# Kernel optimization log

Hardware: AMD Instinct MI355X
Metric: run time of the kernel (lower is better)

The kernel has to match this reference:

```python
import jax, jax.numpy as jnp
from jax import lax
import numpy as np

B, T = 2, 4096
NQ, NAUX, NR, NS, K = 256, 28, 512, 256, 2
DIL = [2 ** i for i in range(10)] * 3  # 30 residual blocks
L = len(DIL)


def _causal_conv(x, w, b, d):
    # x: (B, Cin, T), w: (Cout, Cin, K) -- left-pad (K-1)*d for causality
    pad = (w.shape[-1] - 1) * d
    y = lax.conv_general_dilated(x, w, window_strides=(1,), padding=[(pad, 0)],
                                 rhs_dilation=(d,),
                                 dimension_numbers=('NCH', 'OIH', 'NCH'))
    return y + b[None, :, None]


def _conv1x1(x, w, b):
    # x: (B, Cin, T), w: (Cout, Cin)
    return jnp.einsum('oc,bct->bot', w, x) + b[None, :, None]


def setup_inputs() -> dict:
    key = jax.random.key(0)
    ks = jax.random.split(key, 32)
    s = 0.05
    n = lambda k, shp: (jax.random.normal(k, shp, dtype=jnp.float32) * s)
    return {
        'x': jax.random.randint(ks[0], (B, T), 0, NQ, dtype=jnp.int32),
        'h': jax.random.normal(ks[1], (B, NAUX, T), dtype=jnp.float32),
        'causal_w': n(ks[2], (NR, NQ, K)), 'causal_b': n(ks[3], (NR,)),
        'dil_sig_w': n(ks[4], (L, NR, NR, K)), 'dil_sig_b': n(ks[5], (L, NR)),
        'dil_tanh_w': n(ks[6], (L, NR, NR, K)), 'dil_tanh_b': n(ks[7], (L, NR)),
        'aux_sig_w': n(ks[8], (L, NR, NAUX)), 'aux_sig_b': n(ks[9], (L, NR)),
        'aux_tanh_w': n(ks[10], (L, NR, NAUX)), 'aux_tanh_b': n(ks[11], (L, NR)),
        'skip_w': n(ks[12], (L, NS, NR)), 'skip_b': n(ks[13], (L, NS)),
        'res_w': n(ks[14], (L, NR, NR)), 'res_b': n(ks[15], (L, NR)),
        'post1_w': n(ks[16], (NS, NS)), 'post1_b': n(ks[17], (NS,)),
        'post2_w': n(ks[18], (NQ, NS)), 'post2_b': n(ks[19], (NQ,)),
        'lin_w': n(ks[20], (NQ, NQ)), 'lin_b': n(ks[21], (NQ,)),
    }


def reference(x, h, causal_w, causal_b, dil_sig_w, dil_sig_b, dil_tanh_w,
              dil_tanh_b, aux_sig_w, aux_sig_b, aux_tanh_w, aux_tanh_b,
              skip_w, skip_b, res_w, res_b, post1_w, post1_b, post2_w,
              post2_b, lin_w, lin_b):
    # preprocess: one-hot -> (B, NQ, T) -> causal conv
    oh = jax.nn.one_hot(x % NQ, NQ, dtype=jnp.float32).transpose(0, 2, 1)
    out = _causal_conv(oh, causal_w, causal_b, 1)  # (B, NR, T)
    skip_sum = jnp.zeros((B, NS, T), dtype=jnp.float32)
    for l, d in enumerate(DIL):
        s = _causal_conv(out, dil_sig_w[l], dil_sig_b[l], d) \
            + _conv1x1(h, aux_sig_w[l], aux_sig_b[l])
        t = _causal_conv(out, dil_tanh_w[l], dil_tanh_b[l], d) \
            + _conv1x1(h, aux_tanh_w[l], aux_tanh_b[l])
        g = jax.nn.sigmoid(s) * jnp.tanh(t)  # gated activation (B, NR, T)
        skip_sum = skip_sum + _conv1x1(g, skip_w[l], skip_b[l])
        out = _conv1x1(g, res_w[l], res_b[l]) + out  # residual
    o = jax.nn.relu(skip_sum)
    o = jax.nn.relu(_conv1x1(o, post1_w, post1_b))
    o = _conv1x1(o, post2_w, post2_b).transpose(0, 2, 1)  # (B, T, NQ)
    return o @ lin_w.T + lin_b
```

## Files before the change

kernel.cpp:

```cpp
#include <hip/hip_runtime.h>
#include <cstddef>

#define B_ 2
#define T_ 4096
#define NQ_ 256
#define NAUX_ 28
#define NR_ 512
#define NS_ 256
#define L_ 30

typedef _Float16 half_t;
typedef __attribute__((ext_vector_type(8))) _Float16 f16x8;
typedef __attribute__((ext_vector_type(4))) _Float16 f16x4;
typedef __attribute__((ext_vector_type(4))) float f32x4;

__device__ inline half_t f2h(float f) { return (half_t)f; }
__device__ inline float h2f(half_t h) { return (float)h; }

__device__ __forceinline__ void gload16(const void* g, void* l) {
    __builtin_amdgcn_global_load_lds(
        (const __attribute__((address_space(1))) unsigned int*)g,
        (__attribute__((address_space(3))) unsigned int*)l, 16, 0, 0);
}

__global__ __launch_bounds__(256) void gates_gemm(
    const half_t* __restrict__ actB, const half_t* __restrict__ Wg,
    const float* __restrict__ biasG, half_t* __restrict__ g,
    const half_t* __restrict__ zbuf, int dil)
{
    __shared__ __align__(16) half_t sA[128 * 64];
    __shared__ __align__(16) half_t sB[128 * 64];

    const int tid = threadIdx.x;
    const int b = blockIdx.z;
    const int tB = blockIdx.x * 128;
    const int mB = blockIdx.y * 128;
    const int w = tid >> 6, lane = tid & 63;
    const int wm = w >> 1, wn = w & 1;
    const int l15 = lane & 15, lg = lane >> 4;
    const int rr = lane >> 3, cc = lane & 7;
    const int sc8 = cc ^ rr;

    f32x4 acc[4][4] = {};

    const half_t* Wb = Wg + (size_t)mB * 1088;

    for (int kc = 0; kc < 17; kc++) {
#pragma unroll
        for (int it = 0; it < 4; it++) {
            const int row = w * 32 + it * 8 + rr;
            gload16(Wb + (size_t)row * 1088 + kc * 64 + sc8 * 8,
                    &sA[(w * 32 + it * 8) * 64]);
        }
#pragma unroll
        for (int it = 0; it < 4; it++) {
            const int t = tB + w * 32 + it * 8 + rr;
            const half_t* p;
            if (kc < 8) {
                p = actB + ((size_t)b * T_ + t) * 576 + kc * 64;
            } else if (kc < 16) {
                const int tp = t - dil;
                p = (tp >= 0) ? actB + ((size_t)b * T_ + tp) * 576 + (kc - 8) * 64
                              : zbuf;
            } else {
                p = actB + ((size_t)b * T_ + t) * 576 + 512;
            }
            gload16(p + sc8 * 8, &sB[(w * 32 + it * 8) * 64]);
        }
        __syncthreads();
#pragma unroll
        for (int s = 0; s < 2; s++) {
            f16x8 av[4], bv[4];
#pragma unroll
            for (int i = 0; i < 4; i++) {
                const int r = wm * 64 + i * 16 + l15;
                av[i] = *(const f16x8*)&sA[r * 64 + (((s * 4 + lg) ^ (l15 & 7)) * 8)];
            }
#pragma unroll
            for (int j = 0; j < 4; j++) {
                const int r = wn * 64 + j * 16 + l15;
                bv[j] = *(const f16x8*)&sB[r * 64 + (((s * 4 + lg) ^ (l15 & 7)) * 8)];
            }
#pragma unroll
            for (int i = 0; i < 4; i++)
#pragma unroll
                for (int j = 0; j < 4; j++)
                    acc[i][j] = __builtin_amdgcn_mfma_f32_16x16x32_f16(av[i], bv[j], acc[i][j], 0, 0, 0);
        }
        __syncthreads();
    }

    const int gidx = blockIdx.y * 2 + wm;
    const int t0 = tB + wn * 64 + l15;
#pragma unroll
    for (int i = 0; i < 2; i++) {
        const int c = gidx * 32 + i * 16 + lg * 4;
        const float4 bs = *(const float4*)&biasG[gidx * 64 + i * 16 + lg * 4];
        const float4 bt4 = *(const float4*)&biasG[gidx * 64 + 32 + i * 16 + lg * 4];
        const float bsa[4] = {bs.x, bs.y, bs.z, bs.w};
        const float bta[4] = {bt4.x, bt4.y, bt4.z, bt4.w};
#pragma unroll
        for (int j = 0; j < 4; j++) {
            const int t = t0 + j * 16;
            f16x4 o;
#pragma unroll
            for (int e = 0; e < 4; e++) {
                const float sv = acc[i][j][e] + bsa[e];
                const float tv = acc[i + 2][j][e] + bta[e];
                const float sg = 1.f / (1.f + __expf(-sv));
                const float ex = __expf(-2.f * tv);
                const float th = (1.f - ex) / (1.f + ex);
                o[e] = f2h(sg * th);
            }
            *(f16x4*)(g + ((size_t)b * T_ + t) * 512 + c) = o;
        }
    }
}

template<int EPI>
__global__ __launch_bounds__(256) void gemm_mfma(
    const half_t* __restrict__ X, const half_t* __restrict__ W,
    const float* __restrict__ bias, void* __restrict__ out, int M, int K,
    half_t* __restrict__ actB, half_t* __restrict__ skipH)
{
    __shared__ __align__(16) half_t sA[128 * 64];
    __shared__ __align__(16) half_t sB[128 * 64];

    const int tid = threadIdx.x;
    const int b = blockIdx.z;
    const int tB = blockIdx.x * 128;
    const int mB = blockIdx.y * 128;
    const int w = tid >> 6, lane = tid & 63;
    const int wm = w >> 1, wn = w & 1;
    const int l15 = lane & 15, lg = lane >> 4;
    const int rr = lane >> 3, cc = lane & 7;
    const int sc8 = cc ^ rr;

    f32x4 acc[4][4] = {};

    const half_t* Xb = X + ((size_t)b * T_ + tB) * K;
    const half_t* Wb = W + (size_t)mB * K;

    const int nk = K >> 6;
    for (int kc = 0; kc < nk; kc++) {
        const int k0 = kc << 6;
#pragma unroll
        for (int it = 0; it < 4; it++) {
            const int row = w * 32 + it * 8 + rr;
            gload16(Wb + (size_t)row * K + k0 + sc8 * 8, &sA[(w * 32 + it * 8) * 64]);
            gload16(Xb + (size_t)row * K + k0 + sc8 * 8, &sB[(w * 32 + it * 8) * 64]);
        }
        __syncthreads();
#pragma unroll
        for (int s = 0; s < 2; s++) {
            f16x8 av[4], bv[4];
#pragma unroll
            for (int i = 0; i < 4; i++) {
                const int r = wm * 64 + i * 16 + l15;
                av[i] = *(const f16x8*)&sA[r * 64 + (((s * 4 + lg) ^ (l15 & 7)) * 8)];
            }
#pragma unroll
            for (int j = 0; j < 4; j++) {
                const int r = wn * 64 + j * 16 + l15;
                bv[j] = *(const f16x8*)&sB[r * 64 + (((s * 4 + lg) ^ (l15 & 7)) * 8)];
            }
#pragma unroll
            for (int i = 0; i < 4; i++)
#pragma unroll
                for (int j = 0; j < 4; j++)
                    acc[i][j] = __builtin_amdgcn_mfma_f32_16x16x32_f16(av[i], bv[j], acc[i][j], 0, 0, 0);
        }
        __syncthreads();
    }

    const int n0 = tB + wn * 64 + l15;
#pragma unroll
    for (int i = 0; i < 4; i++) {
        const int m = mB + wm * 64 + i * 16 + lg * 4;
        float4 bv = make_float4(0.f, 0.f, 0.f, 0.f);
        if (bias) bv = *(const float4*)&bias[m];
#pragma unroll
        for (int j = 0; j < 4; j++) {
            const int t = n0 + j * 16;
            float o0 = acc[i][j][0] + bv.x, o1 = acc[i][j][1] + bv.y;
            float o2 = acc[i][j][2] + bv.z, o3 = acc[i][j][3] + bv.w;
            if (EPI == 1) {
                o0 = fmaxf(o0, 0.f); o1 = fmaxf(o1, 0.f);
                o2 = fmaxf(o2, 0.f); o3 = fmaxf(o3, 0.f);
            }
            if (EPI == 3) {
                const size_t bt = (size_t)b * T_ + t;
                half_t* p = (mB < 512) ? (actB + bt * 576 + m)
                                       : (skipH + bt * 256 + (m - 512));
                f16x4 old = *(const f16x4*)p;
                f16x4 nv = {f2h(h2f(old.x) + o0), f2h(h2f(old.y) + o1),
                            f2h(h2f(old.z) + o2), f2h(h2f(old.w) + o3)};
                *(f16x4*)p = nv;
            } else {
                const size_t off = ((size_t)b * T_ + t) * M + m;
                if (EPI == 2) {
                    *(float4*)((float*)out + off) = make_float4(o0, o1, o2, o3);
                } else {
                    f16x4 ov = {f2h(o0), f2h(o1), f2h(o2), f2h(o3)};
                    *(f16x4*)((half_t*)out + off) = ov;
                }
            }
        }
    }
}

__global__ __launch_bounds__(256) void relupack_kernel(
    const half_t* __restrict__ skipH, half_t* __restrict__ outp)
{
    const int idx = blockIdx.x * 256 + threadIdx.x;
    const int c = (idx & 63) * 4;
    const int bt = idx >> 6;
    const f16x4 v = *(const f16x4*)(skipH + (size_t)bt * 256 + c);
    f16x4 o = {f2h(fmaxf(h2f(v.x), 0.f)), f2h(fmaxf(h2f(v.y), 0.f)),
               f2h(fmaxf(h2f(v.z), 0.f)), f2h(fmaxf(h2f(v.w), 0.f))};
    *(f16x4*)(outp + (size_t)bt * 256 + c) = o;
}

__global__ __launch_bounds__(256) void embed_kernel(
    const int* __restrict__ x, const float* __restrict__ cw,
    const float* __restrict__ cb, half_t* __restrict__ actB)
{
    const int t = blockIdx.x, b = blockIdx.y;
    const int idc = x[b * T_ + t];
    const int idp = (t > 0) ? x[b * T_ + t - 1] : -1;
    const size_t bt = (size_t)b * T_ + t;
    for (int c = threadIdx.x; c < 512; c += 256) {
        float v = cw[(c * 256 + idc) * 2 + 1] + cb[c];
        if (idp >= 0) v += cw[(c * 256 + idp) * 2 + 0];
        actB[bt * 576 + c] = f2h(v);
    }
}

__global__ __launch_bounds__(256) void packh_kernel(
    const float* __restrict__ h, half_t* __restrict__ actB)
{
    const int idx = blockIdx.x * 256 + threadIdx.x;
    const int j = idx & 63;
    const int bt = idx >> 6;
    const int b = bt >> 12, t = bt & 4095;
    const float v = (j < 28) ? h[((size_t)b * NAUX_ + j) * T_ + t] : 0.f;
    actB[(size_t)bt * 576 + 512 + j] = f2h(v);
}

__global__ __launch_bounds__(256) void packgate_kernel(
    const float* __restrict__ dsw, const float* __restrict__ dtw,
    half_t* __restrict__ Wg)
{
    const int idx = blockIdx.x * 256 + threadIdx.x;
    const int kg = idx & 63;
    const int r = (idx >> 6) & 1023;
    const int l = idx >> 16;
    const int rsub = r & 63;
    const int c = (r >> 6) * 32 + (rsub & 31);
    const float* src = (rsub < 32) ? dsw : dtw;
    const int k0 = kg * 8;
    const float4* p = (const float4*)(src + (((size_t)l * 512 + c) * 512 + k0) * 2);
    const float4 q0 = p[0], q1 = p[1], q2 = p[2], q3 = p[3];
    f16x8 cur = {f2h(q0.y), f2h(q0.w), f2h(q1.y), f2h(q1.w),
                 f2h(q2.y), f2h(q2.w), f2h(q3.y), f2h(q3.w)};
    f16x8 pst = {f2h(q0.x), f2h(q0.z), f2h(q1.x), f2h(q1.z),
                 f2h(q2.x), f2h(q2.z), f2h(q3.x), f2h(q3.z)};
    half_t* row = Wg + ((size_t)l * 1024 + r) * 1088;
    *(f16x8*)&row[k0] = cur;
    *(f16x8*)&row[512 + k0] = pst;
}

__global__ __launch_bounds__(256) void packgaux_kernel(
    const float* __restrict__ asw, const float* __restrict__ atw,
    half_t* __restrict__ Wg)
{
    const int idx = blockIdx.x * 256 + threadIdx.x;
    const int j8 = idx & 7;
    const int r = (idx >> 3) & 1023;
    const int l = idx >> 13;
    const int rsub = r & 63;
    const int c = (r >> 6) * 32 + (rsub & 31);
    const float* src = (rsub < 32) ? asw : atw;
    f16x8 v = {};
#pragma unroll
    for (int e = 0; e < 8; e++) {
        const int j = j8 * 8 + e;
        if (j < NAUX_) v[e] = f2h(src[((size_t)l * 512 + c) * NAUX_ + j]);
    }
    *(f16x8*)&Wg[((size_t)l * 1024 + r) * 1088 + 1024 + j8 * 8] = v;
}

__global__ __launch_bounds__(256) void packsr_kernel(
    const float* __restrict__ rsw, const float* __restrict__ skw,
    half_t* __restrict__ Wsr)
{
    const int idx = blockIdx.x * 256 + threadIdx.x;
    const int c = (idx & 127) * 4;
    const int r = (idx >> 7) % 768;
    const int l = idx / (128 * 768);
    const float4 v = (r < 512)
        ? *(const float4*)&rsw[((size_t)l * 512 + r) * 512 + c]
        : *(const float4*)&skw[((size_t)l * 256 + (r - 512)) * 512 + c];
    f16x4 o = {f2h(v.x), f2h(v.y), f2h(v.z), f2h(v.w)};
    *(f16x4*)(Wsr + ((size_t)l * 768 + r) * 512 + c) = o;
}

__global__ __launch_bounds__(256) void packpost_kernel(
    const float* __restrict__ p1w, const float* __restrict__ p2w,
    const float* __restrict__ lw, half_t* __restrict__ Wpost)
{
    const int idx = blockIdx.x * 256 + threadIdx.x;
    const int c = (idx & 63) * 4;
    const int r = (idx >> 6) & 255;
    const int mi = idx >> 14;
    const float* src = (mi == 0) ? p1w : (mi == 1) ? p2w : lw;
    const float4 v = *(const float4*)&src[(size_t)r * 256 + c];
    f16x4 o = {f2h(v.x), f2h(v.y), f2h(v.z), f2h(v.w)};
    *(f16x4*)(Wpost + (size_t)mi * 65536 + (size_t)r * 256 + c) = o;
}

__global__ __launch_bounds__(256) void packbias_kernel(
    const float* __restrict__ dsb, const float* __restrict__ asb,
    const float* __restrict__ dtb, const float* __restrict__ atb,
    const float* __restrict__ rsb, const float* __restrict__ skb,
    float* __restrict__ biasG, float* __restrict__ biasSr)
{
    const int idx = blockIdx.x * 256 + threadIdx.x;
    if (idx < 30 * 1024) {
        const int l = idx >> 10, r = idx & 1023;
        const int rsub = r & 63;
        const int c = (r >> 6) * 32 + (rsub & 31);
        const float v = (rsub < 32) ? (dsb[l * 512 + c] + asb[l * 512 + c])
                                    : (dtb[l * 512 + c] + atb[l * 512 + c]);
        biasG[idx] = v;
    } else if (idx < 30 * 1024 + 30 * 768) {
        const int j = idx - 30 * 1024;
        const int l = j / 768, r = j % 768;
        biasSr[j] = (r < 512) ? rsb[l * 512 + r] : skb[l * 256 + (r - 512)];
    }
}

extern "C" void kernel_launch(void* const* d_in, const int* in_sizes, int n_in,
                              void* d_out, int out_size, void* d_ws, size_t ws_size,
                              hipStream_t stream)
{
    (void)in_sizes; (void)n_in; (void)out_size; (void)ws_size;

    const int* x = (const int*)d_in[0];
    const float* h = (const float*)d_in[1];
    const float* causal_w = (const float*)d_in[2];
    const float* causal_b = (const float*)d_in[3];
    const float* dsw = (const float*)d_in[4];
    const float* dsb = (const float*)d_in[5];
    const float* dtw = (const float*)d_in[6];
    const float* dtb = (const float*)d_in[7];
    const float* asw = (const float*)d_in[8];
    const float* asb = (const float*)d_in[9];
    const float* atw = (const float*)d_in[10];
    const float* atb = (const float*)d_in[11];
    const float* skw = (const float*)d_in[12];
    const float* skb = (const float*)d_in[13];
    const float* rsw = (const float*)d_in[14];
    const float* rsb = (const float*)d_in[15];
    const float* p1w = (const float*)d_in[16];
    const float* p1b = (const float*)d_in[17];
    const float* p2w = (const float*)d_in[18];
    const float* p2b = (const float*)d_in[19];
    const float* lw  = (const float*)d_in[20];
    const float* lb  = (const float*)d_in[21];

    char* ws = (char*)d_ws;
    size_t off = 0;
    auto alloc = [&](size_t bytes) { char* p = ws + off; off += (bytes + 255) & ~(size_t)255; return p; };

    half_t* Wg     = (half_t*)alloc((size_t)L_ * 1024 * 1088 * 2);
    half_t* Wsr    = (half_t*)alloc((size_t)L_ * 768 * 512 * 2);
    half_t* Wpost  = (half_t*)alloc((size_t)3 * 256 * 256 * 2);
    float*  biasG  = (float*) alloc((size_t)L_ * 1024 * 4);
    float*  biasSr = (float*) alloc((size_t)L_ * 768 * 4);
    half_t* actB   = (half_t*)alloc((size_t)B_ * T_ * 576 * 2);
    half_t* g      = (half_t*)alloc((size_t)B_ * T_ * 512 * 2);
    half_t* skipH  = (half_t*)alloc((size_t)B_ * T_ * 256 * 2);
    half_t* zbuf   = (half_t*)alloc(256);
    half_t* pA     = (half_t*)alloc((size_t)B_ * T_ * 256 * 2);
    half_t* pB     = (half_t*)alloc((size_t)B_ * T_ * 256 * 2);

    hipMemsetAsync(skipH, 0, (size_t)B_ * T_ * 256 * 2 + 256, stream);

    packgate_kernel<<<30 * 1024 * 64 / 256, 256, 0, stream>>>(dsw, dtw, Wg);
    packgaux_kernel<<<30 * 1024 * 8 / 256, 256, 0, stream>>>(asw, atw, Wg);
    packsr_kernel<<<30 * 768 * 128 / 256, 256, 0, stream>>>(rsw, skw, Wsr);
    packpost_kernel<<<3 * 256 * 64 / 256, 256, 0, stream>>>(p1w, p2w, lw, Wpost);
    packbias_kernel<<<(30 * 1024 + 30 * 768 + 255) / 256, 256, 0, stream>>>(
        dsb, asb, dtb, atb, rsb, skb, biasG, biasSr);
    packh_kernel<<<B_ * T_ * 64 / 256, 256, 0, stream>>>(h, actB);
    embed_kernel<<<dim3(T_, B_), 256, 0, stream>>>(x, causal_w, causal_b, actB);

    for (int l = 0; l < L_; l++) {
        const int dil = 1 << (l % 10);
        gates_gemm<<<dim3(32, 8, B_), 256, 0, stream>>>(
            actB, Wg + (size_t)l * 1024 * 1088, biasG + (size_t)l * 1024, g, zbuf, dil);
        gemm_mfma<3><<<dim3(32, 6, B_), 256, 0, stream>>>(
            g, Wsr + (size_t)l * 768 * 512, biasSr + (size_t)l * 768, nullptr, 768, 512,
            actB, skipH);
    }

    relupack_kernel<<<B_ * T_ * 64 / 256, 256, 0, stream>>>(skipH, pA);
    gemm_mfma<1><<<dim3(32, 2, B_), 256, 0, stream>>>(pA, Wpost, p1b, pB, 256, 256,
                                                      nullptr, nullptr);
    gemm_mfma<0><<<dim3(32, 2, B_), 256, 0, stream>>>(pB, Wpost + 65536, p2b, pA, 256, 256,
                                                      nullptr, nullptr);
    gemm_mfma<2><<<dim3(32, 2, B_), 256, 0, stream>>>(pA, Wpost + 131072, lb, d_out, 256, 256,
                                                      nullptr, nullptr);
}
```

Before: 1.550 ms.

## Pre-pack weights in MFMA fragment order, load A to registers, double-buffer B

Weight matrices are repacked at setup into a per-lane MFMA fragment layout, so each wave loads its A operands straight from global memory into registers with coalesced 16-byte loads. This removes the A tile from LDS entirely. The activation tile in LDS is now double-buffered, with the next chunk's A and B loads issued before the current chunk's compute, giving one sync per k-step and overlap of loads with MFMA. Launch bounds request two blocks per CU, and K becomes a template parameter. The cost is higher register pressure from the two A register sets, plus repeated global reads of weights across blocks that now rely on cache instead of LDS sharing.

Result: no change. 1.524 ms (-1.7%).

```diff
diff --git a/kernel.cpp b/kernel.cpp
--- a/kernel.cpp
+++ b/kernel.cpp
@@ -23,18 +23,17 @@
         (__attribute__((address_space(3))) unsigned int*)l, 16, 0, 0);
 }
 
-__global__ __launch_bounds__(256) void gates_gemm(
-    const half_t* __restrict__ actB, const half_t* __restrict__ Wg,
+
+__global__ __launch_bounds__(256, 2) void gates_gemm(
+    const half_t* __restrict__ actB, const half_t* __restrict__ Wf,
     const float* __restrict__ biasG, half_t* __restrict__ g,
     const half_t* __restrict__ zbuf, int dil)
 {
-    __shared__ __align__(16) half_t sA[128 * 64];
-    __shared__ __align__(16) half_t sB[128 * 64];
+    __shared__ __align__(16) half_t sB[2][128 * 64];
 
     const int tid = threadIdx.x;
     const int b = blockIdx.z;
     const int tB = blockIdx.x * 128;
-    const int mB = blockIdx.y * 128;
     const int w = tid >> 6, lane = tid & 63;
     const int wm = w >> 1, wn = w & 1;
     const int l15 = lane & 15, lg = lane >> 4;
@@ -42,16 +41,18 @@
     const int sc8 = cc ^ rr;
 
     f32x4 acc[4][4] = {};
-
-    const half_t* Wb = Wg + (size_t)mB * 1088;
-
-    for (int kc = 0; kc < 17; kc++) {
-#pragma unroll
-        for (int it = 0; it < 4; it++) {
-            const int row = w * 32 + it * 8 + rr;
-            gload16(Wb + (size_t)row * 1088 + kc * 64 + sc8 * 8,
-                    &sA[(w * 32 + it * 8) * 64]);
-        }
+    f16x8 a0[8], a1[8];
+
+    const int mgW = blockIdx.y * 8 + wm * 4;
+
+    auto loadA = [&](f16x8* d, int kc) {
+#pragma unroll
+        for (int i = 0; i < 4; i++)
+#pragma unroll
+            for (int s = 0; s < 2; s++)
+                d[i * 2 + s] = *(const f16x8*)&Wf[((size_t)(mgW + i) * 34 + kc * 2 + s) * 512 + lane * 8];
+    };
+    auto stageB = [&](int kc, int buf) {
 #pragma unroll
         for (int it = 0; it < 4; it++) {
             const int t = tB + w * 32 + it * 8 + rr;
@@ -65,29 +66,36 @@
             } else {
                 p = actB + ((size_t)b * T_ + t) * 576 + 512;
             }
-            gload16(p + sc8 * 8, &sB[(w * 32 + it * 8) * 64]);
-        }
-        __syncthreads();
+            gload16(p + sc8 * 8, &sB[buf][(w * 32 + it * 8) * 64]);
+        }
+    };
+    auto compute = [&](const f16x8* a, int buf) {
 #pragma unroll
         for (int s = 0; s < 2; s++) {
-            f16x8 av[4], bv[4];
-#pragma unroll
-            for (int i = 0; i < 4; i++) {
-                const int r = wm * 64 + i * 16 + l15;
-                av[i] = *(const f16x8*)&sA[r * 64 + (((s * 4 + lg) ^ (l15 & 7)) * 8)];
-            }
+            f16x8 bv[4];
 #pragma unroll
             for (int j = 0; j < 4; j++) {
                 const int r = wn * 64 + j * 16 + l15;
-                bv[j] = *(const f16x8*)&sB[r * 64 + (((s * 4 + lg) ^ (l15 & 7)) * 8)];
+                bv[j] = *(const f16x8*)&sB[buf][r * 64 + (((s * 4 + lg) ^ (l15 & 7)) * 8)];
             }
 #pragma unroll
             for (int i = 0; i < 4; i++)
 #pragma unroll
                 for (int j = 0; j < 4; j++)
-                    acc[i][j] = __builtin_amdgcn_mfma_f32_16x16x32_f16(av[i], bv[j], acc[i][j], 0, 0, 0);
-        }
+                    acc[i][j] = __builtin_amdgcn_mfma_f32_16x16x32_f16(a[i * 2 + s], bv[j], acc[i][j], 0, 0, 0);
+        }
+    };
+
+    stageB(0, 0);
+    loadA(a0, 0);
+#pragma unroll
+    for (int kc = 0; kc < 17; kc++) {
         __syncthreads();
+        if (kc + 1 < 17) {
+            stageB(kc + 1, (kc + 1) & 1);
+            loadA((kc & 1) ? a0 : a1, kc + 1);
+        }
+        compute((kc & 1) ? a1 : a0, kc & 1);
     }
 
     const int gidx = blockIdx.y * 2 + wm;
@@ -117,14 +125,15 @@
     }
 }
 
-template<int EPI>
-__global__ __launch_bounds__(256) void gemm_mfma(
-    const half_t* __restrict__ X, const half_t* __restrict__ W,
-    const float* __restrict__ bias, void* __restrict__ out, int M, int K,
+template<int K, int EPI>
+__global__ __launch_bounds__(256, 2) void gemm_mfma(
+    const half_t* __restrict__ X, const half_t* __restrict__ Wf,
+    const float* __restrict__ bias, void* __restrict__ out, int M,
     half_t* __restrict__ actB, half_t* __restrict__ skipH)
 {
-    __shared__ __align__(16) half_t sA[128 * 64];
-    __shared__ __align__(16) half_t sB[128 * 64];
+    constexpr int NK = K / 64;
+    constexpr int NKS = K / 32;
+    __shared__ __align__(16) half_t sB[2][128 * 64];
 
     const int tid = threadIdx.x;
     const int b = blockIdx.z;
@@ -137,40 +146,53 @@
     const int sc8 = cc ^ rr;
 
     f32x4 acc[4][4] = {};
-
+    f16x8 a0[8], a1[8];
+
+    const int mgW = (mB >> 4) + wm * 4;
     const half_t* Xb = X + ((size_t)b * T_ + tB) * K;
-    const half_t* Wb = W + (size_t)mB * K;
-
-    const int nk = K >> 6;
-    for (int kc = 0; kc < nk; kc++) {
-        const int k0 = kc << 6;
+
+    auto loadA = [&](f16x8* d, int kc) {
+#pragma unroll
+        for (int i = 0; i < 4; i++)
+#pragma unroll
+            for (int s = 0; s < 2; s++)
+                d[i * 2 + s] = *(const f16x8*)&Wf[((size_t)(mgW + i) * NKS + kc * 2 + s) * 512 + lane * 8];
+    };
+    auto stageB = [&](int kc, int buf) {
 #pragma unroll
         for (int it = 0; it < 4; it++) {
-            const int row = w * 32 + it * 8 + rr;
-            gload16(Wb + (size_t)row * K + k0 + sc8 * 8, &sA[(w * 32 + it * 8) * 64]);
-            gload16(Xb + (size_t)row * K + k0 + sc8 * 8, &sB[(w * 32 + it * 8) * 64]);
-        }
-        __syncthreads();
+            const int row = w * 32 + it * 8;
+            gload16(Xb + (size_t)(row + rr) * K + kc * 64 + sc8 * 8,
+                    &sB[buf][row * 64]);
+        }
+    };
+    auto compute = [&](const f16x8* a, int buf) {
 #pragma unroll
         for (int s = 0; s < 2; s++) {
-            f16x8 av[4], bv[4];
-#pragma unroll
-            for (int i = 0; i < 4; i++) {
-                const int r = wm * 64 + i * 16 + l15;
-                av[i] = *(const f16x8*)&sA[r * 64 + (((s * 4 + lg) ^ (l15 & 7)) * 8)];
-            }
+            f16x8 bv[4];
 #pragma unroll
             for (int j = 0; j < 4; j++) {
                 const int r = wn * 64 + j * 16 + l15;
-                bv[j] = *(const f16x8*)&sB[r * 64 + (((s * 4 + lg) ^ (l15 & 7)) * 8)];
+                bv[j] = *(const f16x8*)&sB[buf][r * 64 + (((s * 4 + lg) ^ (l15 & 7)) * 8)];
             }
 #pragma unroll
             for (int i = 0; i < 4; i++)
 #pragma unroll
                 for (int j = 0; j < 4; j++)
-                    acc[i][j] = __builtin_amdgcn_mfma_f32_16x16x32_f16(av[i], bv[j], acc[i][j], 0, 0, 0);
-        }
+                    acc[i][j] = __builtin_amdgcn_mfma_f32_16x16x32_f16(a[i * 2 + s], bv[j], acc[i][j], 0, 0, 0);
+        }
+    };
+
+    stageB(0, 0);
+    loadA(a0, 0);
+#pragma unroll
+    for (int kc = 0; kc < NK; kc++) {
         __syncthreads();
+        if (kc + 1 < NK) {
+            stageB(kc + 1, (kc + 1) & 1);
+            loadA((kc & 1) ? a0 : a1, kc + 1);
+        }
+        compute((kc & 1) ? a1 : a0, kc & 1);
     }
 
     const int n0 = tB + wn * 64 + l15;
@@ -252,22 +274,24 @@
     half_t* __restrict__ Wg)
 {
     const int idx = blockIdx.x * 256 + threadIdx.x;
-    const int kg = idx & 63;
-    const int r = (idx >> 6) & 1023;
+    const int lane = idx & 63;
+    const int ks = (idx >> 6) & 15;
+    const int mg = (idx >> 10) & 63;
     const int l = idx >> 16;
+    const int r = mg * 16 + (lane & 15);
     const int rsub = r & 63;
     const int c = (r >> 6) * 32 + (rsub & 31);
     const float* src = (rsub < 32) ? dsw : dtw;
-    const int k0 = kg * 8;
-    const float4* p = (const float4*)(src + (((size_t)l * 512 + c) * 512 + k0) * 2);
+    const size_t base = ((size_t)(l * 512 + c) * 512 + ks * 32 + (lane >> 4) * 8) * 2;
+    const float4* p = (const float4*)(src + base);
     const float4 q0 = p[0], q1 = p[1], q2 = p[2], q3 = p[3];
     f16x8 cur = {f2h(q0.y), f2h(q0.w), f2h(q1.y), f2h(q1.w),
                  f2h(q2.y), f2h(q2.w), f2h(q3.y), f2h(q3.w)};
     f16x8 pst = {f2h(q0.x), f2h(q0.z), f2h(q1.x), f2h(q1.z),
                  f2h(q2.x), f2h(q2.z), f2h(q3.x), f2h(q3.z)};
-    half_t* row = Wg + ((size_t)l * 1024 + r) * 1088;
-    *(f16x8*)&row[k0] = cur;
-    *(f16x8*)&row[512 + k0] = pst;
+    half_t* dst = Wg + (size_t)l * 1114112;
+    *(f16x8*)&dst[((size_t)(mg * 34 + ks) * 64 + lane) * 8] = cur;
+    *(f16x8*)&dst[((size_t)(mg * 34 + 16 + ks) * 64 + lane) * 8] = pst;
 }
 
 __global__ __launch_bounds__(256) void packgaux_kernel(
@@ -275,19 +299,23 @@
     half_t* __restrict__ Wg)
 {
     const int idx = blockIdx.x * 256 + threadIdx.x;
-    const int j8 = idx & 7;
-    const int r = (idx >> 3) & 1023;
+    const int lane = idx & 63;
+    const int ksd = (idx >> 6) & 1;
+    const int mg = (idx >> 7) & 63;
     const int l = idx >> 13;
+    const int r = mg * 16 + (lane & 15);
     const int rsub = r & 63;
     const int c = (r >> 6) * 32 + (rsub & 31);
     const float* src = (rsub < 32) ? asw : atw;
+    const int j0 = ksd * 32 + (lane >> 4) * 8;
     f16x8 v = {};
 #pragma unroll
     for (int e = 0; e < 8; e++) {
-        const int j = j8 * 8 + e;
-        if (j < NAUX_) v[e] = f2h(src[((size_t)l * 512 + c) * NAUX_ + j]);
-    }
-    *(f16x8*)&Wg[((size_t)l * 1024 + r) * 1088 + 1024 + j8 * 8] = v;
+        const int j = j0 + e;
+        if (j < NAUX_) v[e] = f2h(src[(size_t)(l * 512 + c) * NAUX_ + j]);
+    }
+    Wg += (size_t)l * 1114112;
+    *(f16x8*)&Wg[((size_t)(mg * 34 + 32 + ksd) * 64 + lane) * 8] = v;
 }
 
 __global__ __launch_bounds__(256) void packsr_kernel(
@@ -295,14 +323,18 @@
     half_t* __restrict__ Wsr)
 {
     const int idx = blockIdx.x * 256 + threadIdx.x;
-    const int c = (idx & 127) * 4;
-    const int r = (idx >> 7) % 768;
-    const int l = idx / (128 * 768);
-    const float4 v = (r < 512)
-        ? *(const float4*)&rsw[((size_t)l * 512 + r) * 512 + c]
-        : *(const float4*)&skw[((size_t)l * 256 + (r - 512)) * 512 + c];
-    f16x4 o = {f2h(v.x), f2h(v.y), f2h(v.z), f2h(v.w)};
-    *(f16x4*)(Wsr + ((size_t)l * 768 + r) * 512 + c) = o;
+    const int lane = idx & 63;
+    const int ks = (idx >> 6) & 15;
+    const int mg = (idx >> 10) % 48;
+    const int l = (idx >> 10) / 48;
+    const int r = mg * 16 + (lane & 15);
+    const int kb = ks * 32 + (lane >> 4) * 8;
+    const float* src = (r < 512) ? (rsw + ((size_t)l * 512 + r) * 512 + kb)
+                                 : (skw + ((size_t)l * 256 + (r - 512)) * 512 + kb);
+    const float4 q0 = ((const float4*)src)[0], q1 = ((const float4*)src)[1];
+    f16x8 v = {f2h(q0.x), f2h(q0.y), f2h(q0.z), f2h(q0.w),
+               f2h(q1.x), f2h(q1.y), f2h(q1.z), f2h(q1.w)};
+    *(f16x8*)&Wsr[(size_t)l * 393216 + ((size_t)(mg * 16 + ks) * 64 + lane) * 8] = v;
 }
 
 __global__ __launch_bounds__(256) void packpost_kernel(
@@ -310,13 +342,18 @@
     const float* __restrict__ lw, half_t* __restrict__ Wpost)
 {
     const int idx = blockIdx.x * 256 + threadIdx.x;
-    const int c = (idx & 63) * 4;
-    const int r = (idx >> 6) & 255;
-    const int mi = idx >> 14;
+    const int lane = idx & 63;
+    const int ks = (idx >> 6) & 7;
+    const int mg = (idx >> 9) & 15;
+    const int mi = idx >> 13;
     const float* src = (mi == 0) ? p1w : (mi == 1) ? p2w : lw;
-    const float4 v = *(const float4*)&src[(size_t)r * 256 + c];
-    f16x4 o = {f2h(v.x), f2h(v.y), f2h(v.z), f2h(v.w)};
-    *(f16x4*)(Wpost + (size_t)mi * 65536 + (size_t)r * 256 + c) = o;
+    const int r = mg * 16 + (lane & 15);
+    const int kb = ks * 32 + (lane >> 4) * 8;
+    const float4 q0 = ((const float4*)(src + (size_t)r * 256 + kb))[0];
+    const float4 q1 = ((const float4*)(src + (size_t)r * 256 + kb))[1];
+    f16x8 v = {f2h(q0.x), f2h(q0.y), f2h(q0.z), f2h(q0.w),
+               f2h(q1.x), f2h(q1.y), f2h(q1.z), f2h(q1.w)};
+    *(f16x8*)&Wpost[(size_t)mi * 65536 + ((size_t)(mg * 8 + ks) * 64 + lane) * 8] = v;
 }
 
 __global__ __launch_bounds__(256) void packbias_kernel(
@@ -373,9 +410,9 @@
     size_t off = 0;
     auto alloc = [&](size_t bytes) { char* p = ws + off; off += (bytes + 255) & ~(size_t)255; return p; };
 
-    half_t* Wg     = (half_t*)alloc((size_t)L_ * 1024 * 1088 * 2);
-    half_t* Wsr    = (half_t*)alloc((size_t)L_ * 768 * 512 * 2);
-    half_t* Wpost  = (half_t*)alloc((size_t)3 * 256 * 256 * 2);
+    half_t* Wg     = (half_t*)alloc((size_t)L_ * 1114112 * 2);
+    half_t* Wsr    = (half_t*)alloc((size_t)L_ * 393216 * 2);
+    half_t* Wpost  = (half_t*)alloc((size_t)3 * 65536 * 2);
     float*  biasG  = (float*) alloc((size_t)L_ * 1024 * 4);
     float*  biasSr = (float*) alloc((size_t)L_ * 768 * 4);
     half_t* actB   = (half_t*)alloc((size_t)B_ * T_ * 576 * 2);
@@ -387,10 +424,10 @@
 
     hipMemsetAsync(skipH, 0, (size_t)B_ * T_ * 256 * 2 + 256, stream);
 
-    packgate_kernel<<<30 * 1024 * 64 / 256, 256, 0, stream>>>(dsw, dtw, Wg);
-    packgaux_kernel<<<30 * 1024 * 8 / 256, 256, 0, stream>>>(asw, atw, Wg);
-    packsr_kernel<<<30 * 768 * 128 / 256, 256, 0, stream>>>(rsw, skw, Wsr);
-    packpost_kernel<<<3 * 256 * 64 / 256, 256, 0, stream>>>(p1w, p2w, lw, Wpost);
+    packgate_kernel<<<30 * 64 * 16 * 64 / 256, 256, 0, stream>>>(dsw, dtw, Wg);
+    packgaux_kernel<<<30 * 64 * 2 * 64 / 256, 256, 0, stream>>>(asw, atw, Wg);
+    packsr_kernel<<<30 * 48 * 16 * 64 / 256, 256, 0, stream>>>(rsw, skw, Wsr);
+    packpost_kernel<<<3 * 16 * 8 * 64 / 256, 256, 0, stream>>>(p1w, p2w, lw, Wpost);
     packbias_kernel<<<(30 * 1024 + 30 * 768 + 255) / 256, 256, 0, stream>>>(
         dsb, asb, dtb, atb, rsb, skb, biasG, biasSr);
     packh_kernel<<<B_ * T_ * 64 / 256, 256, 0, stream>>>(h, actB);
@@ -399,17 +436,17 @@
     for (int l = 0; l < L_; l++) {
         const int dil = 1 << (l % 10);
         gates_gemm<<<dim3(32, 8, B_), 256, 0, stream>>>(
-            actB, Wg + (size_t)l * 1024 * 1088, biasG + (size_t)l * 1024, g, zbuf, dil);
-        gemm_mfma<3><<<dim3(32, 6, B_), 256, 0, stream>>>(
-            g, Wsr + (size_t)l * 768 * 512, biasSr + (size_t)l * 768, nullptr, 768, 512,
+            actB, Wg + (size_t)l * 1114112, biasG + (size_t)l * 1024, g, zbuf, dil);
+        gemm_mfma<512, 3><<<dim3(32, 6, B_), 256, 0, stream>>>(
+            g, Wsr + (size_t)l * 393216, biasSr + (size_t)l * 768, nullptr, 768,
             actB, skipH);
     }
 
     relupack_kernel<<<B_ * T_ * 64 / 256, 256, 0, stream>>>(skipH, pA);
-    gemm_mfma<1><<<dim3(32, 2, B_), 256, 0, stream>>>(pA, Wpost, p1b, pB, 256, 256,
-                                                      nullptr, nullptr);
-    gemm_mfma<0><<<dim3(32, 2, B_), 256, 0, stream>>>(pB, Wpost + 65536, p2b, pA, 256, 256,
-                                                      nullptr, nullptr);
-    gemm_mfma<2><<<dim3(32, 2, B_), 256, 0, stream>>>(pA, Wpost + 131072, lb, d_out, 256, 256,
-                                                      nullptr, nullptr);
-}
+    gemm_mfma<256, 1><<<dim3(32, 2, B_), 256, 0, stream>>>(pA, Wpost, p1b, pB, 256,
+                                                           nullptr, nullptr);
+    gemm_mfma<256, 0><<<dim3(32, 2, B_), 256, 0, stream>>>(pB, Wpost + 65536, p2b, pA, 256,
+                                                           nullptr, nullptr);
+    gemm_mfma<256, 2><<<dim3(32, 2, B_), 256, 0, stream>>>(pA, Wpost + 131072, lb, d_out, 256,
+                                                           nullptr, nullptr);
+}
```
